# Kernel optimization log

Measured on AMD Instinct MI355X. Metric: run time of the kernel, lower is better.

Reference implementation:

```python
import jax, jax.numpy as jnp
import numpy as np

SCALE = 2
PAD = 4
EPS = 1e-5
K = 5
N, C, H, W = 4, 64, 128, 128


def _splits(a, s):
    # (..., W, H) -> (..., W/s, H/s, s*s), block decimation matching torch view/permute
    *lead, Wd, Hd = a.shape
    b = a.reshape(*lead, s, Wd // s, s, Hd // s)
    nl = len(lead)
    b = jnp.transpose(b, tuple(range(nl)) + (nl + 1, nl + 3, nl, nl + 2))
    return b.reshape(*lead, Wd // s, Hd // s, s * s)


def _p2o(psf, Hs, Ws):
    # PSF -> OTF: zero-pad, roll to center at origin, FFT
    kh, kw = psf.shape[-2], psf.shape[-1]
    otf = jnp.zeros(psf.shape[:-2] + (Hs, Ws), psf.dtype).at[..., :kh, :kw].set(psf)
    otf = jnp.roll(otf, (-(kh // 2), -(kw // 2)), axis=(-2, -1))
    return jnp.fft.fftn(otf, axes=(-2, -1))


def _upsample(x, s):
    # s-fold zero-filling upsampler (S^T y)
    n, c, h, w = x.shape
    return jnp.zeros((n, c, h * s, w * s), x.dtype).at[..., ::s, ::s].set(x)


def setup_inputs() -> dict:
    key = jax.random.key(0)
    kx, kw_, _ = jax.random.split(key, 3)
    x = jax.random.normal(kx, (N, C, H, W), dtype=jnp.float32)
    w_raw = jax.random.normal(kw_, (1, C, K, K), dtype=jnp.float32)
    weight = jax.nn.softmax(w_raw.reshape(1, C, -1), axis=-1).reshape(1, C, K, K)
    bias = jnp.zeros((1, C, 1, 1), dtype=jnp.float32)
    return {"x": x, "weight": weight, "bias": bias}


def reference(x, weight, bias):
    s = SCALE
    xp = jnp.pad(x, ((0, 0), (0, 0), (PAD, PAD), (PAD, PAD)), mode="wrap")  # circular
    biaseps = jax.nn.sigmoid(bias - 9.0) + EPS  # (1,C,1,1)
    _, _, h, w = xp.shape
    STy = _upsample(xp, s)  # zero-filled upsample
    # nearest-neighbor interpolate by integer factor s
    xn = jnp.repeat(jnp.repeat(xp, s, axis=-2), s, axis=-1)
    FB = _p2o(weight, h * s, w * s)           # (1,C,hs,ws) complex
    FBC = jnp.conj(FB)
    F2B = jnp.abs(FB) ** 2                     # real
    FBFy = FBC * jnp.fft.fftn(STy, axes=(-2, -1))
    FR = FBFy + jnp.fft.fftn(biaseps * xn, axes=(-2, -1))
    x1 = FB * FR
    FBR = jnp.mean(_splits(x1, s), axis=-1)    # (N,C,h,w) complex
    invW = jnp.mean(_splits(F2B, s), axis=-1)  # (1,C,h,w) real
    invWBR = FBR / (invW + biaseps)
    FCBinvWBR = FBC * jnp.tile(invWBR, (1, 1, s, s))
    FX = (FR - FCBinvWBR) / biaseps
    out = jnp.real(jnp.fft.ifftn(FX, axes=(-2, -1)))
    out = out[..., PAD * s:-PAD * s, PAD * s:-PAD * s]
    return out
```

## Files before the change

kernel.cpp:

```cpp
#include <hip/hip_runtime.h>
#include <math.h>


#define MDIM 136
#define RSCF 140
#define RSC4 70
#define HC   69
#define PLANE_HALF (MDIM*HC)
#define NPLANES 256
#define LDS_BYTES (MDIM*RSC4*16 + 612*8)
#define PI_D 3.14159265358979323846
#define NTH 1024

__device__ __forceinline__ int slot136(int k) { return 17*(k & 7) + (k >> 3); }
__device__ __forceinline__ int slot68(int k)  { return 17*(k & 3) + (k >> 2); }

__device__ __forceinline__ float4 q_add(float4 a, float4 b)
{ return make_float4(a.x+b.x, a.y+b.y, a.z+b.z, a.w+b.w); }
__device__ __forceinline__ float4 q_sub(float4 a, float4 b)
{ return make_float4(a.x-b.x, a.y-b.y, a.z-b.z, a.w-b.w); }
__device__ __forceinline__ float4 q_muli(float4 a, float d)
{ return make_float4(-d*a.y, d*a.x, -d*a.w, d*a.z); }
__device__ __forceinline__ float4 q_scale(float4 a, float s)
{ return make_float4(s*a.x, s*a.y, s*a.z, s*a.w); }
__device__ __forceinline__ float4 q_fma(float4 a, float s, float4 acc)
{ return make_float4(fmaf(a.x,s,acc.x), fmaf(a.y,s,acc.y),
                     fmaf(a.z,s,acc.z), fmaf(a.w,s,acc.w)); }
__device__ __forceinline__ float4 cmul4(float4 q, float2 w)
{ return make_float4(q.x*w.x - q.y*w.y, q.x*w.y + q.y*w.x,
                     q.z*w.x - q.w*w.y, q.z*w.y + q.w*w.x); }

template<int DIR, class F>
__device__ __forceinline__ void dft17_sink(float2* z, int base, int stride, F f)
{
    constexpr float C17[9] = {1.f, 0.93247223f, 0.73900892f, 0.44573836f,
                              0.09226836f, -0.27366299f, -0.60263464f,
                              -0.85021714f, -0.98297310f};
    constexpr float S17[9] = {0.f, 0.36124167f, 0.67369564f, 0.89516329f,
                              0.99573418f, 0.96182564f, 0.79801723f,
                              0.52643216f, 0.18374952f};
    constexpr float d = (DIR > 0) ? 1.f : -1.f;
    float xr[17], xi[17];
#pragma unroll
    for (int n = 0; n < 17; n++) {
        float2 v = z[base + n*stride];
        xr[n] = v.x; xi[n] = v.y;
    }
    float ar[8], ai[8], br[8], bi[8];
#pragma unroll
    for (int n = 1; n <= 8; n++) {
        ar[n-1] = xr[n] + xr[17-n];  ai[n-1] = xi[n] + xi[17-n];
        br[n-1] = xr[n] - xr[17-n];  bi[n-1] = xi[n] - xi[17-n];
    }
    float s0r = xr[0], s0i = xi[0];
#pragma unroll
    for (int n = 0; n < 8; n++) { s0r += ar[n]; s0i += ai[n]; }
    f(0, s0r, s0i);
#pragma unroll
    for (int k = 1; k <= 8; k++) {
        float Pr = xr[0], Pi = xi[0], Qr = 0.f, Qi = 0.f;
#pragma unroll
        for (int n = 1; n <= 8; n++) {
            int m = (k*n) % 17;
            float cc = (m <= 8) ? C17[m] : C17[17-m];
            float ss = (m <= 8) ? S17[m] : -S17[17-m];
            Pr = fmaf(ar[n-1], cc, Pr);
            Pi = fmaf(ai[n-1], cc, Pi);
            Qr = fmaf(br[n-1], ss, Qr);
            Qi = fmaf(bi[n-1], ss, Qi);
        }
        f(k,    Pr - d*Qi, Pi + d*Qr);
        f(17-k, Pr + d*Qi, Pi - d*Qr);
    }
}

template<int DIR>
__device__ __forceinline__ void dft17q(float4* z, int base, int stride)
{
    constexpr float C17[9] = {1.f, 0.93247223f, 0.73900892f, 0.44573836f,
                              0.09226836f, -0.27366299f, -0.60263464f,
                              -0.85021714f, -0.98297310f};
    constexpr float S17[9] = {0.f, 0.36124167f, 0.67369564f, 0.89516329f,
                              0.99573418f, 0.96182564f, 0.79801723f,
                              0.52643216f, 0.18374952f};
    constexpr float d = (DIR > 0) ? 1.f : -1.f;
    float4 x0 = z[base];
    float4 a[8], b[8];
#pragma unroll
    for (int n = 1; n <= 8; n++) {
        float4 u = z[base + n*stride];
        float4 v = z[base + (17-n)*stride];
        a[n-1] = q_add(u, v);
        b[n-1] = q_sub(u, v);
    }
    float4 s0 = x0;
#pragma unroll
    for (int n = 0; n < 8; n++) s0 = q_add(s0, a[n]);
    z[base] = s0;
#pragma unroll
    for (int k = 1; k <= 8; k++) {
        float4 P = x0, Q = make_float4(0.f,0.f,0.f,0.f);
#pragma unroll
        for (int n = 1; n <= 8; n++) {
            int m = (k*n) % 17;
            float cc = (m <= 8) ? C17[m] : C17[17-m];
            float ss = (m <= 8) ? S17[m] : -S17[17-m];
            P = q_fma(a[n-1], cc, P);
            Q = q_fma(b[n-1], ss, Q);
        }
        float4 iq = q_muli(Q, d);
        z[base + k*stride]      = q_add(P, iq);
        z[base + (17-k)*stride] = q_sub(P, iq);
    }
}

template<int DIR>
__device__ __forceinline__ void radix4_tw(float2* z, const float2* t68, int base, int n2,
                                          float2 Z0, float2 Z1, float2 Z2, float2 Z3)
{
    constexpr float d = (DIR > 0) ? 1.0f : -1.0f;
    float t0r = Z0.x+Z2.x, t0i = Z0.y+Z2.y;
    float t1r = Z0.x-Z2.x, t1i = Z0.y-Z2.y;
    float t2r = Z1.x+Z3.x, t2i = Z1.y+Z3.y;
    float t3r = Z1.x-Z3.x, t3i = Z1.y-Z3.y;
    float X0r = t0r+t2r,     X0i = t0i+t2i;
    float X2r = t0r-t2r,     X2i = t0i-t2i;
    float X1r = t1r - d*t3i, X1i = t1i + d*t3r;
    float X3r = t1r + d*t3i, X3i = t1i - d*t3r;
    z[base + n2] = make_float2(X0r, X0i);
    float2 w1 = t68[n2], w2 = t68[17 + n2], w3 = t68[34 + n2];
    z[base + 17 + n2] = make_float2(X1r*w1.x - X1i*w1.y, X1r*w1.y + X1i*w1.x);
    z[base + 34 + n2] = make_float2(X2r*w2.x - X2i*w2.y, X2r*w2.y + X2i*w2.x);
    z[base + 51 + n2] = make_float2(X3r*w3.x - X3i*w3.y, X3r*w3.y + X3i*w3.x);
}

template<int DIR>
__device__ __forceinline__ void radix4q_tw(float4* z, const float2* t68, int base, int n2,
                                           float4 Z0, float4 Z1, float4 Z2, float4 Z3)
{
    constexpr float d = (DIR > 0) ? 1.0f : -1.0f;
    float4 t0 = q_add(Z0, Z2), t1 = q_sub(Z0, Z2);
    float4 t2 = q_add(Z1, Z3), t3 = q_sub(Z1, Z3);
    float4 X0 = q_add(t0, t2), X2 = q_sub(t0, t2);
    float4 it3 = q_muli(t3, d);
    float4 X1 = q_add(t1, it3), X3 = q_sub(t1, it3);
    z[base + n2] = X0;
    float2 w1 = t68[n2], w2 = t68[17 + n2], w3 = t68[34 + n2];
    z[base + 17 + n2] = cmul4(X1, w1);
    z[base + 34 + n2] = cmul4(X2, w2);
    z[base + 51 + n2] = cmul4(X3, w3);
}

template<int DIR>
__device__ __forceinline__ void fft136_s1_body(float2* z, const float2* t136,
                                               int c, int n2)
{
    constexpr float d = (DIR > 0) ? 1.0f : -1.0f;
    constexpr float C707 = 0.70710678118654752f;
    float xr[8], xi[8];
#pragma unroll
    for (int n1 = 0; n1 < 8; n1++) {
        float2 v = z[(17*n1 + n2)*RSCF + c];
        xr[n1] = v.x; xi[n1] = v.y;
    }
    float e0r = xr[0]+xr[4], e0i = xi[0]+xi[4];
    float e1r = xr[0]-xr[4], e1i = xi[0]-xi[4];
    float o0r = xr[2]+xr[6], o0i = xi[2]+xi[6];
    float o1r = xr[2]-xr[6], o1i = xi[2]-xi[6];
    float E0r = e0r+o0r, E0i = e0i+o0i;
    float E2r = e0r-o0r, E2i = e0i-o0i;
    float E1r = e1r - d*o1i, E1i = e1i + d*o1r;
    float E3r = e1r + d*o1i, E3i = e1i - d*o1r;
    float f0r = xr[1]+xr[5], f0i = xi[1]+xi[5];
    float f1r = xr[1]-xr[5], f1i = xi[1]-xi[5];
    float h0r = xr[3]+xr[7], h0i = xi[3]+xi[7];
    float h1r = xr[3]-xr[7], h1i = xi[3]-xi[7];
    float O0r = f0r+h0r, O0i = f0i+h0i;
    float O2r = f0r-h0r, O2i = f0i-h0i;
    float O1r = f1r - d*h1i, O1i = f1i + d*h1r;
    float O3r = f1r + d*h1i, O3i = f1i - d*h1r;
    float t1r =  C707*(O1r - d*O1i), t1i = C707*(O1i + d*O1r);
    float t2r = -d*O2i,              t2i = d*O2r;
    float t3r = -C707*(O3r + d*O3i), t3i = C707*(d*O3r - O3i);
    float Xr[8], Xi[8];
    Xr[0]=E0r+O0r; Xi[0]=E0i+O0i;  Xr[4]=E0r-O0r; Xi[4]=E0i-O0i;
    Xr[1]=E1r+t1r; Xi[1]=E1i+t1i;  Xr[5]=E1r-t1r; Xi[5]=E1i-t1i;
    Xr[2]=E2r+t2r; Xi[2]=E2i+t2i;  Xr[6]=E2r-t2r; Xi[6]=E2i-t2i;
    Xr[3]=E3r+t3r; Xi[3]=E3i+t3i;  Xr[7]=E3r-t3r; Xi[7]=E3i-t3i;
    z[n2*RSCF + c] = make_float2(Xr[0], Xi[0]);
#pragma unroll
    for (int k1 = 1; k1 < 8; k1++) {
        float2 w = t136[(k1-1)*17 + n2];
        z[(17*k1 + n2)*RSCF + c] = make_float2(Xr[k1]*w.x - Xi[k1]*w.y,
                                               Xr[k1]*w.y + Xi[k1]*w.x);
    }
}

template<int DIR>
__device__ __forceinline__ void fft136q_s1_body(float4* z, const float2* t136,
                                                int c, int n2)
{
    constexpr float d = (DIR > 0) ? 1.0f : -1.0f;
    constexpr float C707 = 0.70710678118654752f;
    float4 x[8];
#pragma unroll
    for (int n1 = 0; n1 < 8; n1++) x[n1] = z[(17*n1 + n2)*RSC4 + c];
    float4 e0 = q_add(x[0], x[4]), e1 = q_sub(x[0], x[4]);
    float4 o0 = q_add(x[2], x[6]), o1 = q_sub(x[2], x[6]);
    float4 E0 = q_add(e0, o0), E2 = q_sub(e0, o0);
    float4 io1 = q_muli(o1, d);
    float4 E1 = q_add(e1, io1), E3 = q_sub(e1, io1);
    float4 f0 = q_add(x[1], x[5]), f1 = q_sub(x[1], x[5]);
    float4 h0 = q_add(x[3], x[7]), h1 = q_sub(x[3], x[7]);
    float4 O0 = q_add(f0, h0), O2 = q_sub(f0, h0);
    float4 ih1 = q_muli(h1, d);
    float4 O1 = q_add(f1, ih1), O3 = q_sub(f1, ih1);
    float4 t1 = q_scale(q_add(O1, q_muli(O1, d)), C707);
    float4 t2 = q_muli(O2, d);
    float4 t3 = q_scale(q_sub(O3, q_muli(O3, d)), -C707);
    float4 X0 = q_add(E0, O0), X4 = q_sub(E0, O0);
    float4 X1 = q_add(E1, t1), X5 = q_sub(E1, t1);
    float4 X2 = q_add(E2, t2), X6 = q_sub(E2, t2);
    float4 X3 = q_add(E3, t3), X7 = q_sub(E3, t3);
    z[n2*RSC4 + c] = X0;
    z[(17*1 + n2)*RSC4 + c] = cmul4(X1, t136[0*17 + n2]);
    z[(17*2 + n2)*RSC4 + c] = cmul4(X2, t136[1*17 + n2]);
    z[(17*3 + n2)*RSC4 + c] = cmul4(X3, t136[2*17 + n2]);
    z[(17*4 + n2)*RSC4 + c] = cmul4(X4, t136[3*17 + n2]);
    z[(17*5 + n2)*RSC4 + c] = cmul4(X5, t136[4*17 + n2]);
    z[(17*6 + n2)*RSC4 + c] = cmul4(X6, t136[5*17 + n2]);
    z[(17*7 + n2)*RSC4 + c] = cmul4(X7, t136[6*17 + n2]);
}

__device__ __forceinline__ float2 c2r_pack(float2 a, float2 b, float2 w)
{
    float Sr = a.x + b.x, Si = a.y - b.y;
    float Dr = a.x - b.x, Di = a.y + b.y;
    float Or = w.x*Dr - w.y*Di, Oi = w.x*Di + w.y*Dr;
    return make_float2(Sr - Oi, Si + Or);
}
__device__ __forceinline__ float4 c2r_pack4(float4 a, float4 b, float2 w)
{
    float Sx = a.x + b.x, Sy = a.y - b.y;
    float Dx = a.x - b.x, Dy = a.y + b.y;
    float Ox = w.x*Dx - w.y*Dy, Oy = w.x*Dy + w.y*Dx;
    float Sz = a.z + b.z, Sw = a.w - b.w;
    float Dz = a.z - b.z, Dw = a.w + b.w;
    float Oz = w.x*Dz - w.y*Dw, Ow = w.x*Dw + w.y*Dz;
    return make_float4(Sx - Oy, Sy + Ox, Sz - Ow, Sw + Oz);
}

__global__ __launch_bounds__(1024, 4) void conv_kernel(const float* __restrict__ x,
                                                       const float4* __restrict__ Abuf,
                                                       float* __restrict__ out)
{
    extern __shared__ float4 z4s[];
    float4* z4    = z4s;
    float2* zf    = (float2*)z4s;
    float2* lutI  = (float2*)(z4s + MDIM*RSC4);
    float2* lutF  = lutI + MDIM;
    float2* tI136 = lutF + MDIM;
    float2* tF136 = tI136 + 119;
    float2* tI68  = tF136 + 119;
    float2* tF68  = tI68 + 51;
    const int tid = threadIdx.x;
    const int nc  = blockIdx.x;
    const int c   = nc & 63;

    if (tid < MDIM) {
        float s, cc; sincosf(2.0f*(float)PI_D*(float)tid/136.0f, &s, &cc);
        lutI[tid] = make_float2(cc, s);
        lutF[tid] = make_float2(cc, -s);
    } else if (tid < MDIM + 119) {
        int it = tid - MDIM;
        int k1 = it/17 + 1, n2 = it - (it/17)*17;
        float s, cc; sincosf((float)(PI_D/68.0)*(float)(k1*n2), &s, &cc);
        tI136[it] = make_float2(cc, s);
        tF136[it] = make_float2(cc, -s);
    } else if (tid < MDIM + 119 + 51) {
        int it = tid - MDIM - 119;
        int j = it/17, n2 = it - 17*j;
        float s, cc; sincosf((float)(PI_D/34.0)*(float)((j+1)*n2), &s, &cc);
        tI68[it] = make_float2(cc, s);
        tF68[it] = make_float2(cc, -s);
    }
    const float* xp = x + (size_t)nc * (128*128);
    {
        int i = tid / 68, n = tid - (tid/68)*68;
        for (int e = tid; e < MDIM*68; e += NTH) {
            int si = (i + 124) & 127;
            int j0 = (2*n + 124) & 127;
            zf[i*RSCF + n] = *reinterpret_cast<const float2*>(xp + si*128 + j0);
            i += 15; n += 4; if (n >= 68) { n -= 68; i++; }
        }
    }
    __syncthreads();
    {
        int row = tid / 17;
        int n2  = tid - row*17;
        for (int e = tid; e < MDIM*17; e += NTH) {
            int base = row*RSCF;
            float2 Z0 = zf[base + n2];
            float2 Z1 = zf[base + 17 + n2];
            float2 Z2 = zf[base + 34 + n2];
            float2 Z3 = zf[base + 51 + n2];
            radix4_tw<-1>(zf, tF68, base, n2, Z0, Z1, Z2, Z3);
            row += 60; n2 += 4; if (n2 >= 17) { n2 -= 17; row++; }
        }
    }
    __syncthreads();
    if (tid < MDIM*4) {
        int row = tid >> 2, k1 = tid & 3;
        int base = row*RSCF + 17*k1;
        dft17_sink<-1>(zf, base, 1, [&](int k2, float re, float im) {
            zf[base + k2] = make_float2(re, im);
        });
    }
    __syncthreads();
    {
        int row = tid / 35, k = tid - (tid/35)*35;
        for (int e = tid; e < MDIM*35; e += NTH) {
            int base = row*RSCF;
            int sa = slot68(k);
            float2 Za = zf[base+sa];
            float Zar = Za.x, Zai = Za.y;
            float Zbr, Zbi; int sb;
            if (k == 0) { Zbr = Zar; Zbi = Zai; sb = 68; }
            else {
                int kk = 68-k; sb = slot68(kk);
                float2 Zb = zf[base+sb]; Zbr = Zb.x; Zbi = Zb.y;
            }
            float2 w = lutF[k];
            float wc = w.x, ws = w.y;
            float Er = 0.5f*(Zar + Zbr), Ei = 0.5f*(Zai - Zbi);
            float Dr = 0.5f*(Zar - Zbr), Di = 0.5f*(Zai + Zbi);
            float Tr = wc*Dr - ws*Di, Ti = wc*Di + ws*Dr;
            zf[base+sa] = make_float2(Er + Ti, Ei - Tr);
            float E2r = Er,  E2i = -Ei;
            float D2r = -Dr, D2i = Di;
            float w2c = -wc, w2s = ws;
            float T2r = w2c*D2r - w2s*D2i, T2i = w2c*D2i + w2s*D2r;
            zf[base+sb] = make_float2(E2r + T2i, E2i - T2r);
            row += 29; k += 9; if (k >= 35) { k -= 35; row++; }
        }
    }
    __syncthreads();
    for (int e = tid; e < HC*17; e += NTH) {
        int cc = (e*241) >> 12;
        int n2 = e - cc*17;
        fft136_s1_body<-1>(zf, tF136, cc, n2);
    }
    __syncthreads();
    if (tid < HC*8) {
        int cc = tid >> 3, k1 = tid & 7;
        int base = 17*k1*RSCF + cc;
        dft17_sink<-1>(zf, base, RSCF, [&](int k2, float re, float im) {
            zf[base + k2*RSCF] = make_float2(re, im);
        });
    }
    __syncthreads();
    float2 Xreg[10];
    {
        int g1 = tid / HC, g2 = tid - (tid/HC)*HC;
#pragma unroll
        for (int k = 0; k < 10; k++) {
            if (k < 9 || tid < PLANE_HALF - 9*NTH) {
                int cq = (g2 == 68) ? 68 : slot68(g2);
                Xreg[k] = zf[slot136(g1)*RSCF + cq];
            }
            g1 += 14; g2 += 58; if (g2 >= HC) { g2 -= HC; g1++; }
        }
    }
    __syncthreads();
    float* op = out + (size_t)nc * (256*256);
#pragma unroll 1
    for (int u = 0; u < 2; u++) {
        const float4* Ap = Abuf + (size_t)(c*2 + u) * PLANE_HALF;
        {
            int g1 = tid / HC, g2 = tid - (tid/HC)*HC;
#pragma unroll
            for (int k = 0; k < 10; k++) {
                if (k < 9 || tid < PLANE_HALF - 9*NTH) {
                    float2 xv = Xreg[k];
                    float4 av = Ap[tid + k*NTH];
                    z4[g1*RSC4 + g2] = make_float4(
                        av.x*xv.x - av.y*xv.y, av.x*xv.y + av.y*xv.x,
                        av.z*xv.x - av.w*xv.y, av.z*xv.y + av.w*xv.x);
                }
                g1 += 14; g2 += 58; if (g2 >= HC) { g2 -= HC; g1++; }
            }
        }
        __syncthreads();
        for (int e = tid; e < HC*17; e += NTH) {
            int cc = (e*241) >> 12;
            int n2 = e - cc*17;
            fft136q_s1_body<1>(z4, tI136, cc, n2);
        }
        __syncthreads();
        if (tid < HC*8) {
            int cc = tid >> 3, k1 = tid & 7;
            dft17q<1>(z4, 17*k1*RSC4 + cc, RSC4);
        }
        __syncthreads();
        for (int it = tid; it < MDIM*9; it += NTH) {
            int row = (it*7282) >> 16;
            int g   = it - row*9;
            int base = row*RSC4;
            if (g == 0) {
                float4 T0  = z4[base],    T17 = z4[base+17], T34 = z4[base+34],
                       T51 = z4[base+51], T68 = z4[base+68];
                float4 Z0 = c2r_pack4(T0,  T68, lutI[0]);
                float4 Z1 = c2r_pack4(T17, T51, lutI[17]);
                float4 Z2 = c2r_pack4(T34, T34, lutI[34]);
                float4 Z3 = c2r_pack4(T51, T17, lutI[51]);
                radix4q_tw<1>(z4, tI68, base, 0, Z0, Z1, Z2, Z3);
            } else {
                int gb = 17 - g;
                float4 Ta0 = z4[base+g],    Ta1 = z4[base+g+17],
                       Ta2 = z4[base+g+34], Ta3 = z4[base+g+51];
                float4 Tb0 = z4[base+gb],    Tb1 = z4[base+gb+17],
                       Tb2 = z4[base+gb+34], Tb3 = z4[base+gb+51];
                float4 Za0 = c2r_pack4(Ta0, Tb3, lutI[g]);
                float4 Za1 = c2r_pack4(Ta1, Tb2, lutI[g+17]);
                float4 Za2 = c2r_pack4(Ta2, Tb1, lutI[g+34]);
                float4 Za3 = c2r_pack4(Ta3, Tb0, lutI[g+51]);
                float4 Zb0 = c2r_pack4(Tb0, Ta3, lutI[gb]);
                float4 Zb1 = c2r_pack4(Tb1, Ta2, lutI[gb+17]);
                float4 Zb2 = c2r_pack4(Tb2, Ta1, lutI[gb+34]);
                float4 Zb3 = c2r_pack4(Tb3, Ta0, lutI[gb+51]);
                radix4q_tw<1>(z4, tI68, base, g,  Za0, Za1, Za2, Za3);
                radix4q_tw<1>(z4, tI68, base, gb, Zb0, Zb1, Zb2, Zb3);
            }
        }
        __syncthreads();
        if (tid < MDIM*4) {
            int row = tid >> 2, k1 = tid & 3;
            dft17q<1>(z4, row*RSC4 + 17*k1, 1);
        }
        __syncthreads();
        {
            int m  = 2 + (tid & 63);
            int y1 = 4 + (tid >> 6);
            int a  = slot136(y1)*RSC4 + slot68(m);
            float* rowp = op + (size_t)(2*y1 + u - 8)*256 + 4*m - 8;
#pragma unroll
            for (int it = 0; it < 8; ++it) {
                float4 w = z4[a];
                *reinterpret_cast<float4*>(rowp) = make_float4(w.x, w.z, w.y, w.w);
                a += 2*RSC4;
                rowp += 32*256;
            }
        }
        __syncthreads();
    }
}

__global__ void prep_kernel(const float* __restrict__ weight,
                            const float* __restrict__ bias,
                            float4* __restrict__ Abuf)
{
    __shared__ float tabc[272], tabs[272];
    __shared__ float Rs[69*5*4];
    for (int t = threadIdx.x; t < 272; t += blockDim.x) {
        float s, c; sincosf(-2.0f*(float)PI_D*(float)t/272.0f, &s, &c);
        tabc[t] = c; tabs[t] = s;
    }
    const int c     = blockIdx.x >> 3;
    const int chunk = blockIdx.x & 7;
    const float* wp = weight + c*25;
    const float r = 1.0f/(1.0f + expf(9.0f - bias[c])) + 1e-5f;
    __syncthreads();
    for (int it = threadIdx.x; it < 69*5; it += blockDim.x) {
        int g2 = it / 5, a = it - 5*g2;
        float c2 = tabc[g2], s2 = tabs[g2];
        float e2r[5], e2i[5];
        e2r[2]=1.0f; e2i[2]=0.0f; e2r[3]=c2; e2i[3]=s2;
        e2r[4]=c2*c2-s2*s2; e2i[4]=2.0f*c2*s2;
        e2r[1]=c2; e2i[1]=-s2; e2r[0]=e2r[4]; e2i[0]=-e2i[4];
        float w0=wp[a*5+0], w1=wp[a*5+1], w2=wp[a*5+2], w3=wp[a*5+3], w4=wp[a*5+4];
        float Rer = w0*e2r[0] + w2*e2r[2] + w4*e2r[4];
        float Rei = w0*e2i[0] + w2*e2i[2] + w4*e2i[4];
        float Ror = w1*e2r[1] + w3*e2r[3];
        float Roi = w1*e2i[1] + w3*e2i[3];
        Rs[it*4+0] = Rer + Ror;  Rs[it*4+1] = Rei + Roi;
        Rs[it*4+2] = Rer - Ror;  Rs[it*4+3] = Rei - Roi;
    }
    __syncthreads();

    const int e_lo = chunk * 1173;
    const int e_hi = e_lo + 1173;
    int e  = e_lo + (int)threadIdx.x;
    int g1 = e / HC, g2 = e - (e/HC)*HC;
    for (; e < e_hi; e += blockDim.x) {
        float c1 = tabc[g1], s1 = tabs[g1];
        float e1r[5], e1i[5];
        e1r[2]=1.0f; e1i[2]=0.0f; e1r[3]=c1; e1i[3]=s1;
        e1r[4]=c1*c1-s1*s1; e1i[4]=2.0f*c1*s1;
        e1r[1]=c1; e1i[1]=-s1; e1r[0]=e1r[4]; e1i[0]=-e1i[4];

        float FBr[2][2], FBi[2][2];
#pragma unroll
        for (int b1 = 0; b1 < 2; b1++) {
            float Per=0.f, Pei=0.f, Por=0.f, Poi=0.f;
#pragma unroll
            for (int a = 0; a < 5; a++) {
                float Rr = Rs[(g2*5+a)*4 + 2*b1];
                float Ri = Rs[(g2*5+a)*4 + 2*b1 + 1];
                float tr = e1r[a]*Rr - e1i[a]*Ri;
                float ti = e1r[a]*Ri + e1i[a]*Rr;
                if (a & 1) { Por += tr; Poi += ti; } else { Per += tr; Pei += ti; }
            }
            FBr[0][b1] = Per + Por;  FBi[0][b1] = Pei + Poi;
            FBr[1][b1] = Per - Por;  FBi[1][b1] = Pei - Poi;
        }
        float c2 = tabc[g2], s2 = tabs[g2];
        float ur[2]={1.0f+c1, 1.0f-c1}, ui[2]={s1, -s1};
        float vr[2]={1.0f+c2, 1.0f-c2}, vi[2]={s2, -s2};
        float Br_[2][2], Bi_[2][2];
#pragma unroll
        for (int a1 = 0; a1 < 2; a1++)
#pragma unroll
            for (int b1 = 0; b1 < 2; b1++) {
                Br_[a1][b1] = ur[a1]*vr[b1] - ui[a1]*vi[b1];
                Bi_[a1][b1] = ur[a1]*vi[b1] + ui[a1]*vr[b1];
            }
        float invW=0.f, Qr=0.f, Qi=0.f;
#pragma unroll
        for (int a1 = 0; a1 < 2; a1++)
#pragma unroll
            for (int b1 = 0; b1 < 2; b1++) {
                invW += FBr[a1][b1]*FBr[a1][b1] + FBi[a1][b1]*FBi[a1][b1];
                Qr += FBr[a1][b1]*Br_[a1][b1] - FBi[a1][b1]*Bi_[a1][b1];
                Qi += FBr[a1][b1]*Bi_[a1][b1] + FBi[a1][b1]*Br_[a1][b1];
            }
        invW *= 0.25f; Qr *= 0.25f; Qi *= 0.25f;
        float den = 1.0f/(invW + r);
        float Sr = (1.0f - Qr)*den, Si = -Qi*den;
        float Mr[2][2], Mi[2][2];
#pragma unroll
        for (int a1 = 0; a1 < 2; a1++)
#pragma unroll
            for (int b1 = 0; b1 < 2; b1++) {
                Mr[a1][b1] = Br_[a1][b1] + FBr[a1][b1]*Sr + FBi[a1][b1]*Si;
                Mi[a1][b1] = Bi_[a1][b1] + FBr[a1][b1]*Si - FBi[a1][b1]*Sr;
            }
        const float scale = 1.0f/73984.0f;
#pragma unroll
        for (int uu = 0; uu < 2; uu++) {
            float ov[4];
#pragma unroll
            for (int vv = 0; vv < 2; vv++) {
                float sr=0.f, si=0.f;
#pragma unroll
                for (int a1 = 0; a1 < 2; a1++)
#pragma unroll
                    for (int b1 = 0; b1 < 2; b1++) {
                        if ((a1*uu + b1*vv) & 1) { sr -= Mr[a1][b1]; si -= Mi[a1][b1]; }
                        else                     { sr += Mr[a1][b1]; si += Mi[a1][b1]; }
                    }
                int t = g1*uu + g2*vv;
                float pc = tabc[t], ps = -tabs[t];
                ov[2*vv]   = (pc*sr - ps*si)*scale;
                ov[2*vv+1] = (pc*si + ps*sr)*scale;
            }
            Abuf[((size_t)(c*2 + uu))*PLANE_HALF + e] =
                make_float4(ov[0], ov[1], ov[2], ov[3]);
        }
        g1 += 3; g2 += 49; if (g2 >= HC) { g2 -= HC; g1++; }
    }
}

extern "C" void kernel_launch(void* const* d_in, const int* in_sizes, int n_in,
                              void* d_out, int out_size, void* d_ws, size_t ws_size,
                              hipStream_t stream)
{
    const float* x      = (const float*)d_in[0];
    const float* weight = (const float*)d_in[1];
    const float* bias   = (const float*)d_in[2];
    float* out = (float*)d_out;

    float4* Abuf = (float4*)d_ws;

    (void)hipFuncSetAttribute((const void*)conv_kernel,
                              hipFuncAttributeMaxDynamicSharedMemorySize,
                              (int)LDS_BYTES);

    prep_kernel<<<512, 256, 0, stream>>>(weight, bias, Abuf);
    conv_kernel<<<NPLANES, 1024, LDS_BYTES, stream>>>(x, Abuf, out);
}
```

Measured before the change: 140.2 us.

## Keep forward DFT17 outputs in registers and apply spectral multiply directly

The final forward DFT-17 stage now keeps its 17 outputs in registers instead of writing them to LDS. The per-plane multiply then reads the filter buffer at the matching (row, column) positions and writes products straight into the inverse-FFT buffer, which removes one LDS round trip and one barrier. The separate forward twiddle tables are dropped in favour of conjugating the inverse tables, and the LDS row strides change (140→146, 70→73), likely to reduce bank conflicts. The cost is that only 552 threads do the multiply, with strided global reads of the filter buffer.

```diff
diff --git a/kernel.cpp b/kernel.cpp
--- a/kernel.cpp
+++ b/kernel.cpp
@@ -3,12 +3,12 @@
 
 
 #define MDIM 136
-#define RSCF 140
-#define RSC4 70
+#define RSCF 146
+#define RSC4 73
 #define HC   69
 #define PLANE_HALF (MDIM*HC)
 #define NPLANES 256
-#define LDS_BYTES (MDIM*RSC4*16 + 612*8)
+#define LDS_BYTES (MDIM*RSC4*16 + 306*8)
 #define PI_D 3.14159265358979323846
 #define NTH 1024
 
@@ -129,6 +129,7 @@
     float X3r = t1r + d*t3i, X3i = t1i - d*t3r;
     z[base + n2] = make_float2(X0r, X0i);
     float2 w1 = t68[n2], w2 = t68[17 + n2], w3 = t68[34 + n2];
+    if (DIR < 0) { w1.y = -w1.y; w2.y = -w2.y; w3.y = -w3.y; }
     z[base + 17 + n2] = make_float2(X1r*w1.x - X1i*w1.y, X1r*w1.y + X1i*w1.x);
     z[base + 34 + n2] = make_float2(X2r*w2.x - X2i*w2.y, X2r*w2.y + X2i*w2.x);
     z[base + 51 + n2] = make_float2(X3r*w3.x - X3i*w3.y, X3r*w3.y + X3i*w3.x);
@@ -191,6 +192,7 @@
 #pragma unroll
     for (int k1 = 1; k1 < 8; k1++) {
         float2 w = t136[(k1-1)*17 + n2];
+        if (DIR < 0) w.y = -w.y;
         z[(17*k1 + n2)*RSCF + c] = make_float2(Xr[k1]*w.x - Xi[k1]*w.y,
                                                Xr[k1]*w.y + Xi[k1]*w.x);
     }
@@ -232,13 +234,6 @@
     z[(17*7 + n2)*RSC4 + c] = cmul4(X7, t136[6*17 + n2]);
 }
 
-__device__ __forceinline__ float2 c2r_pack(float2 a, float2 b, float2 w)
-{
-    float Sr = a.x + b.x, Si = a.y - b.y;
-    float Dr = a.x - b.x, Di = a.y + b.y;
-    float Or = w.x*Dr - w.y*Di, Oi = w.x*Di + w.y*Dr;
-    return make_float2(Sr - Oi, Si + Or);
-}
 __device__ __forceinline__ float4 c2r_pack4(float4 a, float4 b, float2 w)
 {
     float Sx = a.x + b.x, Sy = a.y - b.y;
@@ -258,11 +253,8 @@
     float4* z4    = z4s;
     float2* zf    = (float2*)z4s;
     float2* lutI  = (float2*)(z4s + MDIM*RSC4);
-    float2* lutF  = lutI + MDIM;
-    float2* tI136 = lutF + MDIM;
-    float2* tF136 = tI136 + 119;
-    float2* tI68  = tF136 + 119;
-    float2* tF68  = tI68 + 51;
+    float2* tI136 = lutI + MDIM;
+    float2* tI68  = tI136 + 119;
     const int tid = threadIdx.x;
     const int nc  = blockIdx.x;
     const int c   = nc & 63;
@@ -270,19 +262,16 @@
     if (tid < MDIM) {
         float s, cc; sincosf(2.0f*(float)PI_D*(float)tid/136.0f, &s, &cc);
         lutI[tid] = make_float2(cc, s);
-        lutF[tid] = make_float2(cc, -s);
     } else if (tid < MDIM + 119) {
         int it = tid - MDIM;
         int k1 = it/17 + 1, n2 = it - (it/17)*17;
         float s, cc; sincosf((float)(PI_D/68.0)*(float)(k1*n2), &s, &cc);
         tI136[it] = make_float2(cc, s);
-        tF136[it] = make_float2(cc, -s);
     } else if (tid < MDIM + 119 + 51) {
         int it = tid - MDIM - 119;
         int j = it/17, n2 = it - 17*j;
         float s, cc; sincosf((float)(PI_D/34.0)*(float)((j+1)*n2), &s, &cc);
         tI68[it] = make_float2(cc, s);
-        tF68[it] = make_float2(cc, -s);
     }
     const float* xp = x + (size_t)nc * (128*128);
     {
@@ -304,7 +293,7 @@
             float2 Z1 = zf[base + 17 + n2];
             float2 Z2 = zf[base + 34 + n2];
             float2 Z3 = zf[base + 51 + n2];
-            radix4_tw<-1>(zf, tF68, base, n2, Z0, Z1, Z2, Z3);
+            radix4_tw<-1>(zf, tI68, base, n2, Z0, Z1, Z2, Z3);
             row += 60; n2 += 4; if (n2 >= 17) { n2 -= 17; row++; }
         }
     }
@@ -330,8 +319,8 @@
                 int kk = 68-k; sb = slot68(kk);
                 float2 Zb = zf[base+sb]; Zbr = Zb.x; Zbi = Zb.y;
             }
-            float2 w = lutF[k];
-            float wc = w.x, ws = w.y;
+            float2 w = lutI[k];
+            float wc = w.x, ws = -w.y;
             float Er = 0.5f*(Zar + Zbr), Ei = 0.5f*(Zai - Zbi);
             float Dr = 0.5f*(Zar - Zbr), Di = 0.5f*(Zai + Zbi);
             float Tr = wc*Dr - ws*Di, Ti = wc*Di + ws*Dr;
@@ -348,46 +337,34 @@
     for (int e = tid; e < HC*17; e += NTH) {
         int cc = (e*241) >> 12;
         int n2 = e - cc*17;
-        fft136_s1_body<-1>(zf, tF136, cc, n2);
-    }
-    __syncthreads();
+        fft136_s1_body<-1>(zf, tI136, cc, n2);
+    }
+    __syncthreads();
+    float2 Xk[17];
+    int g2n = 0, k1S = 0;
     if (tid < HC*8) {
-        int cc = tid >> 3, k1 = tid & 7;
-        int base = 17*k1*RSCF + cc;
-        dft17_sink<-1>(zf, base, RSCF, [&](int k2, float re, float im) {
-            zf[base + k2*RSCF] = make_float2(re, im);
+        int cS = tid >> 3; k1S = tid & 7;
+        int cd = (cS*241) >> 12;
+        int cm = cS - 17*cd;
+        g2n = (cS == 68) ? 68 : (4*cm + cd);
+        dft17_sink<-1>(zf, 17*k1S*RSCF + cS, RSCF, [&](int k2, float re, float im) {
+            Xk[k2] = make_float2(re, im);
         });
-    }
-    __syncthreads();
-    float2 Xreg[10];
-    {
-        int g1 = tid / HC, g2 = tid - (tid/HC)*HC;
-#pragma unroll
-        for (int k = 0; k < 10; k++) {
-            if (k < 9 || tid < PLANE_HALF - 9*NTH) {
-                int cq = (g2 == 68) ? 68 : slot68(g2);
-                Xreg[k] = zf[slot136(g1)*RSCF + cq];
-            }
-            g1 += 14; g2 += 58; if (g2 >= HC) { g2 -= HC; g1++; }
-        }
     }
     __syncthreads();
     float* op = out + (size_t)nc * (256*256);
 #pragma unroll 1
     for (int u = 0; u < 2; u++) {
-        const float4* Ap = Abuf + (size_t)(c*2 + u) * PLANE_HALF;
-        {
-            int g1 = tid / HC, g2 = tid - (tid/HC)*HC;
-#pragma unroll
-            for (int k = 0; k < 10; k++) {
-                if (k < 9 || tid < PLANE_HALF - 9*NTH) {
-                    float2 xv = Xreg[k];
-                    float4 av = Ap[tid + k*NTH];
-                    z4[g1*RSC4 + g2] = make_float4(
-                        av.x*xv.x - av.y*xv.y, av.x*xv.y + av.y*xv.x,
-                        av.z*xv.x - av.w*xv.y, av.z*xv.y + av.w*xv.x);
-                }
-                g1 += 14; g2 += 58; if (g2 >= HC) { g2 -= HC; g1++; }
+        if (tid < HC*8) {
+            const float4* Ag = Abuf + (size_t)(c*2 + u) * PLANE_HALF + g2n;
+#pragma unroll
+            for (int k2 = 0; k2 < 17; k2++) {
+                int g1 = k1S + 8*k2;
+                float4 av = Ag[(size_t)g1*HC];
+                float2 xv = Xk[k2];
+                z4[g1*RSC4 + g2n] = make_float4(
+                    av.x*xv.x - av.y*xv.y, av.x*xv.y + av.y*xv.x,
+                    av.z*xv.x - av.w*xv.y, av.z*xv.y + av.w*xv.x);
             }
         }
         __syncthreads();
```

Measured after the change: 184.9 us. 1.32x slower.
